# Kernel tuning notes

Hardware: AMD Instinct MI355X
Metric: run time of the kernel (lower is better)

Reference implementation:

```python
import jax, jax.numpy as jnp
import numpy as np

DIM = 1024
NUM_EXPERTS = 8
TOP_K = 2
HIDDEN = DIM * 2
B, S = 2, 4096


def setup_inputs() -> dict:
    key = jax.random.key(0)
    ks = jax.random.split(key, 8)
    sd = 1.0 / np.sqrt(DIM)
    sh = 1.0 / np.sqrt(HIDDEN)
    return {
        "x": jax.random.normal(ks[0], (B, S, DIM), dtype=jnp.float32),
        "gate_w": jax.random.uniform(ks[1], (NUM_EXPERTS, DIM), jnp.float32, -sd, sd),
        "gate_b": jax.random.uniform(ks[2], (NUM_EXPERTS,), jnp.float32, -sd, sd),
        "W1": jax.random.uniform(ks[3], (NUM_EXPERTS, DIM, HIDDEN), jnp.float32, -sd, sd),
        "b1": jax.random.uniform(ks[4], (NUM_EXPERTS, HIDDEN), jnp.float32, -sd, sd),
        "W2": jax.random.uniform(ks[5], (NUM_EXPERTS, HIDDEN, DIM), jnp.float32, -sh, sh),
        "b2": jax.random.uniform(ks[6], (NUM_EXPERTS, DIM), jnp.float32, -sh, sh),
    }


def reference(x, gate_w, gate_b, W1, b1, W2, b2):
    Bd, Sd, D = x.shape
    xf = x.reshape(-1, D)                                  # [T, D]
    T = xf.shape[0]
    logits = xf @ gate_w.T + gate_b                        # [T, E]
    weights = jax.nn.softmax(logits.astype(jnp.float32), axis=-1)
    topk_w, topk_i = jax.lax.top_k(weights, TOP_K)         # [T, K]
    topk_w = topk_w / topk_w.sum(axis=-1, keepdims=True)
    # combine weights scattered back to dense [T, E] (top-k indices are distinct)
    comb = jnp.zeros((T, NUM_EXPERTS), topk_w.dtype)
    comb = comb.at[jnp.arange(T)[:, None], topk_i].add(topk_w)
    # dense all-expert FFN (exact GELU, matching nn.GELU default)
    h = jax.nn.gelu(jnp.einsum('td,edh->eth', xf, W1) + b1[:, None, :], approximate=False)
    y = jnp.einsum('eth,ehd->etd', h, W2) + b2[:, None, :]  # [E, T, D]
    out = jnp.einsum('etd,te->td', y, comb.astype(y.dtype)).reshape(Bd, Sd, D)
    return out, logits
```

## Files before the change

### kernel.cpp

```cpp
#include <hip/hip_runtime.h>
#include <math.h>

#define T_TOK 8192
#define DIMX 1024
#define NE 8
#define HID 2048
#define NPAIR (T_TOK * 2)
#define P_PAD (NPAIR + NE * 128)
#define GATE_TPB 32

typedef __attribute__((ext_vector_type(8))) short s16x8;
typedef __attribute__((ext_vector_type(4))) float f32x4;

static __device__ __forceinline__ unsigned short f2bf(float f) {
    union { float f; unsigned u; } v; v.f = f;
    unsigned r = v.u + 0x7FFFu + ((v.u >> 16) & 1u);
    return (unsigned short)(r >> 16);
}
static __device__ __forceinline__ float bf2f(unsigned short u) {
    union { unsigned u; float f; } v; v.u = (unsigned)u << 16; return v.f;
}

static __device__ __forceinline__ float gelu_fast(float v) {
    float u2 = -1.5957691216057308f * v * (1.f + 0.044715f * v * v);
    return v * __builtin_amdgcn_rcpf(1.f + __expf(u2));
}

static __device__ __forceinline__ void gload16(const unsigned short* g, unsigned short* l) {
    __builtin_amdgcn_global_load_lds(
        (const __attribute__((address_space(1))) unsigned int*)g,
        (__attribute__((address_space(3))) unsigned int*)l, 16, 0, 0);
}

__global__ void init_routing_kernel(int* slot_token, float* slot_weight, int* counts) {
    int i = blockIdx.x * blockDim.x + threadIdx.x;
    if (i < P_PAD) { slot_token[i] = 0; slot_weight[i] = 0.f; }
    if (i < NE) counts[i] = 0;
}

__global__ void convx_kernel(const float* __restrict__ x, unsigned short* __restrict__ xb) {
    int i = blockIdx.x * blockDim.x + threadIdx.x;
    float4 f = ((const float4*)x)[i];
    unsigned short r[4] = { f2bf(f.x), f2bf(f.y), f2bf(f.z), f2bf(f.w) };
    *(uint2*)&xb[(size_t)i * 4] = *(const uint2*)&r[0];
}

__global__ __launch_bounds__(256) void conv_transpose_kernel(
    const float* __restrict__ src, unsigned short* __restrict__ dst, int R, int C) {
    __shared__ float tile[64][65];
    int e = blockIdx.z;
    int r0 = blockIdx.y * 64, c0 = blockIdx.x * 64;
    const float* s = src + (size_t)e * R * C;
    unsigned short* d = dst + (size_t)e * R * C;
    int tid = threadIdx.x;
    int lr = tid >> 4, lc4 = (tid & 15) * 4;
    #pragma unroll
    for (int it = 0; it < 4; it++) {
        float4 v = *(const float4*)&s[(size_t)(r0 + it * 16 + lr) * C + c0 + lc4];
        tile[it * 16 + lr][lc4 + 0] = v.x;
        tile[it * 16 + lr][lc4 + 1] = v.y;
        tile[it * 16 + lr][lc4 + 2] = v.z;
        tile[it * 16 + lr][lc4 + 3] = v.w;
    }
    __syncthreads();
    int cc = tid >> 3, rch = (tid & 7) * 8;
    #pragma unroll
    for (int it = 0; it < 2; it++) {
        int c = it * 32 + cc;
        unsigned short r[8];
        #pragma unroll
        for (int j = 0; j < 8; j++) r[j] = f2bf(tile[rch + j][c]);
        *(uint4*)&d[(size_t)(c0 + c) * R + r0 + rch] = *(const uint4*)&r[0];
    }
}

__global__ __launch_bounds__(256) void gate_kernel(
    const float* __restrict__ x, const float* __restrict__ gw, const float* __restrict__ gb,
    float* __restrict__ logits_out, int* counts, int* __restrict__ pair_epos,
    float* __restrict__ pair_w) {
    __shared__ float sgw[NE * DIMX];
    __shared__ int lcount[NE], lbase[NE];
    __shared__ int s_e[GATE_TPB * 2];
    __shared__ int s_lp[GATE_TPB * 2];
    __shared__ float s_wv[GATE_TPB * 2];
    int tid = threadIdx.x;
    for (int i = tid; i < NE * DIMX / 4; i += 256)
        ((float4*)sgw)[i] = ((const float4*)gw)[i];
    if (tid < NE) lcount[tid] = 0;
    __syncthreads();

    int wave = tid >> 6, lane = tid & 63;
    int tbase = blockIdx.x * GATE_TPB;
    for (int r = 0; r < GATE_TPB / 4; ++r) {
        int ti = wave * (GATE_TPB / 4) + r;
        int t = tbase + ti;
        const float* xr = x + (size_t)t * DIMX;
        float acc[NE] = {};
        #pragma unroll
        for (int i = 0; i < DIMX / 256; i++) {
            float4 xv = *(const float4*)&xr[i * 256 + lane * 4];
            #pragma unroll
            for (int e = 0; e < NE; e++) {
                float4 wv = *(const float4*)&sgw[e * DIMX + i * 256 + lane * 4];
                acc[e] += xv.x * wv.x + xv.y * wv.y + xv.z * wv.z + xv.w * wv.w;
            }
        }
        #pragma unroll
        for (int e = 0; e < NE; e++) {
            #pragma unroll
            for (int off = 32; off; off >>= 1) acc[e] += __shfl_xor(acc[e], off);
        }
        if (lane == 0) {
            float* lo = logits_out + (size_t)t * NE;
            #pragma unroll
            for (int e = 0; e < NE; e++) { acc[e] += gb[e]; lo[e] = acc[e]; }
            float l0 = acc[0]; int e0 = 0;
            #pragma unroll
            for (int e = 1; e < NE; e++) if (acc[e] > l0) { l0 = acc[e]; e0 = e; }
            float l1 = -1e30f; int e1 = -1;
            #pragma unroll
            for (int e = 0; e < NE; e++) if (e != e0 && acc[e] > l1) { l1 = acc[e]; e1 = e; }
            float q = expf(l1 - l0);
            float wn0 = 1.f / (1.f + q);
            float wn1 = q / (1.f + q);
            int lp0 = atomicAdd(&lcount[e0], 1);
            int lp1 = atomicAdd(&lcount[e1], 1);
            s_e[ti * 2] = e0; s_lp[ti * 2] = lp0; s_wv[ti * 2] = wn0;
            s_e[ti * 2 + 1] = e1; s_lp[ti * 2 + 1] = lp1; s_wv[ti * 2 + 1] = wn1;
        }
    }
    __syncthreads();
    if (tid < NE) lbase[tid] = atomicAdd(&counts[tid], lcount[tid]);
    __syncthreads();
    if (tid < GATE_TPB * 2) {
        int e = s_e[tid];
        int gp = lbase[e] + s_lp[tid];
        int gi = (tbase + (tid >> 1)) * 2 + (tid & 1);
        pair_epos[gi] = (e << 28) | gp;
        pair_w[gi] = s_wv[tid];
    }
}

__global__ void scan_kernel(const int* counts, int* offsets) {
    if (threadIdx.x == 0 && blockIdx.x == 0) {
        int o = 0;
        offsets[0] = 0;
        for (int e = 0; e < NE; e++) { o += (counts[e] + 127) & ~127; offsets[e + 1] = o; }
    }
}

__global__ void place_kernel(const int* __restrict__ pair_epos, const float* __restrict__ pair_w,
                             const int* __restrict__ offsets, int* __restrict__ slot_token,
                             float* __restrict__ slot_weight, int* __restrict__ tok2slot) {
    int p = blockIdx.x * 256 + threadIdx.x;
    if (p >= NPAIR) return;
    int ep = pair_epos[p];
    int e = ep >> 28;
    int pos = ep & 0x0FFFFFFF;
    int slot = offsets[e] + pos;
    slot_token[slot] = p >> 1;
    slot_weight[slot] = pair_w[p];
    tok2slot[p] = slot;
}

#define BARRIER() asm volatile("s_barrier" ::: "memory")
#define WAIT_VM(n) asm volatile("s_waitcnt vmcnt(" #n ")" ::: "memory")
#define WAIT_LGKM0() do { asm volatile("s_waitcnt lgkmcnt(0)" ::: "memory"); \
                          __builtin_amdgcn_sched_barrier(0); } while (0)


__global__ __launch_bounds__(256) void gemm1_kernel(
    const unsigned short* __restrict__ xb, const unsigned short* __restrict__ W1t,
    const float* __restrict__ b1, const int* __restrict__ offsets,
    const int* __restrict__ slot_token, unsigned short* __restrict__ hbuf) {
    int e = blockIdx.x;
    int row_base = offsets[e];
    int rows = offsets[e + 1] - row_base;
    int m0 = blockIdx.z * 128;
    if (m0 >= rows) return;
    int n0 = blockIdx.y * 128;

    __shared__ unsigned short sA[3][128 * 32];
    __shared__ unsigned short sB[3][128 * 32];

    int tid = threadIdx.x;
    const unsigned short* w1e = W1t + (size_t)e * HID * DIMX;

    int srow = tid >> 2;
    int kperm = (tid & 3) ^ ((tid >> 3) & 3);
    int tok0 = slot_token[row_base + m0 + srow];
    int tok1 = slot_token[row_base + m0 + srow + 64];
    const unsigned short* gA0 = xb + (size_t)tok0 * DIMX + kperm * 8;
    const unsigned short* gA1 = xb + (size_t)tok1 * DIMX + kperm * 8;
    const unsigned short* gB0 = w1e + (size_t)(n0 + srow) * DIMX + kperm * 8;
    const unsigned short* gB1 = w1e + (size_t)(n0 + srow + 64) * DIMX + kperm * 8;

#define STG1(b, k0) do { \
        gload16(gA0 + (k0), &sA[b][tid * 8]); \
        gload16(gA1 + (k0), &sA[b][(tid + 256) * 8]); \
        gload16(gB0 + (k0), &sB[b][tid * 8]); \
        gload16(gB1 + (k0), &sB[b][(tid + 256) * 8]); \
    } while (0)

    f32x4 acc[4][4] = {};
    int wv = tid >> 6; int wr = wv >> 1, wc = wv & 1;
    int lane = tid & 63; int lr = lane & 15, lg = lane >> 4;
    int kx8 = (lg ^ ((lr >> 1) & 3)) * 8;

#define CMP1(CUR) do { \
        s16x8 af[4], bfr[4]; \
        _Pragma("unroll") \
        for (int m = 0; m < 4; m++) af[m] = *(const s16x8*)&sA[CUR][(wr * 64 + m * 16 + lr) * 32 + kx8]; \
        _Pragma("unroll") \
        for (int n = 0; n < 4; n++) bfr[n] = *(const s16x8*)&sB[CUR][(wc * 64 + n * 16 + lr) * 32 + kx8]; \
        __builtin_amdgcn_s_setprio(1); \
        _Pragma("unroll") \
        for (int m = 0; m < 4; m++) { \
            _Pragma("unroll") \
            for (int n = 0; n < 4; n++) \
                acc[m][n] = __builtin_amdgcn_mfma_f32_16x16x32_bf16(af[m], bfr[n], acc[m][n], 0, 0, 0); \
        } \
        __builtin_amdgcn_s_setprio(0); \
    } while (0)

    const int NT = DIMX / 32;
    STG1(0, 0);
    STG1(1, 32);
    int cur = 0;
    for (int t = 0; t < NT - 2; ++t) {
        int nxt = cur + 2; if (nxt >= 3) nxt -= 3;
        STG1(nxt, (t + 2) * 32);
        WAIT_VM(8);
        BARRIER();
        CMP1(cur);
        WAIT_LGKM0();
        BARRIER();
        cur = (cur + 1 == 3) ? 0 : cur + 1;
    }
    WAIT_VM(4);
    BARRIER();
    CMP1(cur);
    WAIT_LGKM0();
    BARRIER();
    cur = (cur + 1 == 3) ? 0 : cur + 1;
    WAIT_VM(0);
    BARRIER();
    CMP1(cur);
#undef STG1
#undef CMP1

    #pragma unroll
    for (int m = 0; m < 4; m++) {
        #pragma unroll
        for (int n = 0; n < 4; n++) {
            int col = n0 + wc * 64 + n * 16 + lr;
            float bias = b1[e * HID + col];
            #pragma unroll
            for (int i = 0; i < 4; i++) {
                int row = wr * 64 + m * 16 + lg * 4 + i;
                float v = gelu_fast(acc[m][n][i] + bias);
                hbuf[(size_t)(row_base + m0 + row) * HID + col] = f2bf(v);
            }
        }
    }
}

__global__ __launch_bounds__(256) void gemm2_kernel(
    const unsigned short* __restrict__ hbuf, const unsigned short* __restrict__ W2t,
    const float* __restrict__ b2, const int* __restrict__ offsets,
    const float* __restrict__ slot_weight, unsigned short* __restrict__ ybuf) {
    int e = blockIdx.x;
    int row_base = offsets[e];
    int rows = offsets[e + 1] - row_base;
    int m0 = blockIdx.z * 128;
    if (m0 >= rows) return;
    int n0 = blockIdx.y * 128;

    __shared__ unsigned short sA[3][128 * 32];
    __shared__ unsigned short sB[3][128 * 32];
    __shared__ float s_w[128];

    int tid = threadIdx.x;
    if (tid < 128) s_w[tid] = slot_weight[row_base + m0 + tid];

    const unsigned short* ha = hbuf + (size_t)(row_base + m0) * HID;
    const unsigned short* w2e = W2t + (size_t)e * DIMX * HID;

    int srow = tid >> 2;
    int kperm = (tid & 3) ^ ((tid >> 3) & 3);
    const unsigned short* gA0 = ha + (size_t)srow * HID + kperm * 8;
    const unsigned short* gA1 = ha + (size_t)(srow + 64) * HID + kperm * 8;
    const unsigned short* gB0 = w2e + (size_t)(n0 + srow) * HID + kperm * 8;
    const unsigned short* gB1 = w2e + (size_t)(n0 + srow + 64) * HID + kperm * 8;

#define STG2(b, k0) do { \
        gload16(gA0 + (k0), &sA[b][tid * 8]); \
        gload16(gA1 + (k0), &sA[b][(tid + 256) * 8]); \
        gload16(gB0 + (k0), &sB[b][tid * 8]); \
        gload16(gB1 + (k0), &sB[b][(tid + 256) * 8]); \
    } while (0)

    f32x4 acc[4][4] = {};
    int wv = tid >> 6; int wr = wv >> 1, wc = wv & 1;
    int lane = tid & 63; int lr = lane & 15, lg = lane >> 4;
    int kx8 = (lg ^ ((lr >> 1) & 3)) * 8;

#define CMP2(CUR) do { \
        s16x8 af[4], bfr[4]; \
        _Pragma("unroll") \
        for (int m = 0; m < 4; m++) af[m] = *(const s16x8*)&sA[CUR][(wr * 64 + m * 16 + lr) * 32 + kx8]; \
        _Pragma("unroll") \
        for (int n = 0; n < 4; n++) bfr[n] = *(const s16x8*)&sB[CUR][(wc * 64 + n * 16 + lr) * 32 + kx8]; \
        __builtin_amdgcn_s_setprio(1); \
        _Pragma("unroll") \
        for (int m = 0; m < 4; m++) { \
            _Pragma("unroll") \
            for (int n = 0; n < 4; n++) \
                acc[m][n] = __builtin_amdgcn_mfma_f32_16x16x32_bf16(af[m], bfr[n], acc[m][n], 0, 0, 0); \
        } \
        __builtin_amdgcn_s_setprio(0); \
    } while (0)

    const int NT = HID / 32;
    STG2(0, 0);
    STG2(1, 32);
    int cur = 0;
    for (int t = 0; t < NT - 2; ++t) {
        int nxt = cur + 2; if (nxt >= 3) nxt -= 3;
        STG2(nxt, (t + 2) * 32);
        WAIT_VM(8);
        BARRIER();
        CMP2(cur);
        WAIT_LGKM0();
        BARRIER();
        cur = (cur + 1 == 3) ? 0 : cur + 1;
    }
    WAIT_VM(4);
    BARRIER();
    CMP2(cur);
    WAIT_LGKM0();
    BARRIER();
    cur = (cur + 1 == 3) ? 0 : cur + 1;
    WAIT_VM(0);
    BARRIER();
    CMP2(cur);
#undef STG2
#undef CMP2

    #pragma unroll
    for (int m = 0; m < 4; m++) {
        #pragma unroll
        for (int n = 0; n < 4; n++) {
            int col = n0 + wc * 64 + n * 16 + lr;
            float bias = b2[e * DIMX + col];
            #pragma unroll
            for (int i = 0; i < 4; i++) {
                int row = wr * 64 + m * 16 + lg * 4 + i;
                float v = (acc[m][n][i] + bias) * s_w[row];
                ybuf[(size_t)(row_base + m0 + row) * DIMX + col] = f2bf(v);
            }
        }
    }
}

__global__ __launch_bounds__(256) void combine_kernel(
    const unsigned short* __restrict__ ybuf, const int* __restrict__ tok2slot,
    float* __restrict__ out) {
    int t = blockIdx.x;
    int d = threadIdx.x * 4;
    int sa = tok2slot[t * 2], sb = tok2slot[t * 2 + 1];
    ushort4 a = *(const ushort4*)&ybuf[(size_t)sa * DIMX + d];
    ushort4 b = *(const ushort4*)&ybuf[(size_t)sb * DIMX + d];
    float4 o;
    o.x = bf2f(a.x) + bf2f(b.x);
    o.y = bf2f(a.y) + bf2f(b.y);
    o.z = bf2f(a.z) + bf2f(b.z);
    o.w = bf2f(a.w) + bf2f(b.w);
    *(float4*)&out[(size_t)t * DIMX + d] = o;
}

extern "C" void kernel_launch(void* const* d_in, const int* in_sizes, int n_in,
                              void* d_out, int out_size, void* d_ws, size_t ws_size,
                              hipStream_t stream) {
    const float* x  = (const float*)d_in[0];
    const float* gw = (const float*)d_in[1];
    const float* gb = (const float*)d_in[2];
    const float* W1 = (const float*)d_in[3];
    const float* b1 = (const float*)d_in[4];
    const float* W2 = (const float*)d_in[5];
    const float* b2 = (const float*)d_in[6];
    float* out = (float*)d_out;
    float* logits = out + (size_t)T_TOK * DIMX;

    char* ws = (char*)d_ws;
    unsigned short* W2t = (unsigned short*)ws; ws += (size_t)NE * DIMX * HID * 2;
    unsigned short* W1t = (unsigned short*)ws;
    unsigned short* ybuf = (unsigned short*)ws; ws += (size_t)NE * DIMX * HID * 2;
    unsigned short* xb = (unsigned short*)ws; ws += (size_t)T_TOK * DIMX * 2;
    unsigned short* hbuf = (unsigned short*)ws; ws += (size_t)P_PAD * HID * 2;
    int* counts = (int*)ws; ws += 256;
    int* offsets = (int*)ws; ws += 256;
    int* pair_epos = (int*)ws; ws += (size_t)NPAIR * 4;
    float* pair_w = (float*)ws; ws += (size_t)NPAIR * 4;
    int* slot_token = (int*)ws; ws += (size_t)P_PAD * 4;
    float* slot_weight = (float*)ws; ws += (size_t)P_PAD * 4;
    int* tok2slot = (int*)ws; ws += (size_t)NPAIR * 4;

    init_routing_kernel<<<(P_PAD + 255) / 256, 256, 0, stream>>>(slot_token, slot_weight, counts);
    convx_kernel<<<T_TOK * DIMX / 4 / 256, 256, 0, stream>>>(x, xb);
    conv_transpose_kernel<<<dim3(HID / 64, DIMX / 64, NE), 256, 0, stream>>>(W1, W1t, DIMX, HID);
    conv_transpose_kernel<<<dim3(DIMX / 64, HID / 64, NE), 256, 0, stream>>>(W2, W2t, HID, DIMX);
    gate_kernel<<<T_TOK / GATE_TPB, 256, 0, stream>>>(x, gw, gb, logits, counts, pair_epos, pair_w);
    scan_kernel<<<1, 1, 0, stream>>>(counts, offsets);
    place_kernel<<<NPAIR / 256, 256, 0, stream>>>(pair_epos, pair_w, offsets, slot_token,
                                                  slot_weight, tok2slot);
    gemm1_kernel<<<dim3(NE, HID / 128, 128), 256, 0, stream>>>(xb, W1t, b1, offsets, slot_token, hbuf);
    gemm2_kernel<<<dim3(NE, DIMX / 128, 128), 256, 0, stream>>>(hbuf, W2t, b2, offsets, slot_weight, ybuf);
    combine_kernel<<<T_TOK, 256, 0, stream>>>(ybuf, tok2slot, out);
}
```

Measured before the change: 285.4 us.

## Fuse x bf16 conversion into gate kernel and use double-buffered GEMM pipelines

The separate x-to-bf16 conversion kernel is removed; the gate kernel now writes the bf16 copy of x while it already reads x for the gating dot products, saving one launch and one full read of x. Both expert GEMM kernels go from a 3-stage LDS pipeline (two tiles prefetched ahead) to a 2-stage double buffer. That shrinks LDS use, which may allow more resident blocks, but each tile load has less time to hide its latency.

After: 281.0 us. Within noise of the previous version (-1.5%).

```diff
diff --git a/kernel.cpp b/kernel.cpp
--- a/kernel.cpp
+++ b/kernel.cpp
@@ -36,13 +36,6 @@
     int i = blockIdx.x * blockDim.x + threadIdx.x;
     if (i < P_PAD) { slot_token[i] = 0; slot_weight[i] = 0.f; }
     if (i < NE) counts[i] = 0;
-}
-
-__global__ void convx_kernel(const float* __restrict__ x, unsigned short* __restrict__ xb) {
-    int i = blockIdx.x * blockDim.x + threadIdx.x;
-    float4 f = ((const float4*)x)[i];
-    unsigned short r[4] = { f2bf(f.x), f2bf(f.y), f2bf(f.z), f2bf(f.w) };
-    *(uint2*)&xb[(size_t)i * 4] = *(const uint2*)&r[0];
 }
 
 __global__ __launch_bounds__(256) void conv_transpose_kernel(
@@ -77,7 +70,7 @@
 __global__ __launch_bounds__(256) void gate_kernel(
     const float* __restrict__ x, const float* __restrict__ gw, const float* __restrict__ gb,
     float* __restrict__ logits_out, int* counts, int* __restrict__ pair_epos,
-    float* __restrict__ pair_w) {
+    float* __restrict__ pair_w, unsigned short* __restrict__ xb) {
     __shared__ float sgw[NE * DIMX];
     __shared__ int lcount[NE], lbase[NE];
     __shared__ int s_e[GATE_TPB * 2];
@@ -99,6 +92,8 @@
         #pragma unroll
         for (int i = 0; i < DIMX / 256; i++) {
             float4 xv = *(const float4*)&xr[i * 256 + lane * 4];
+            unsigned short rb[4] = { f2bf(xv.x), f2bf(xv.y), f2bf(xv.z), f2bf(xv.w) };
+            *(uint2*)&xb[(size_t)t * DIMX + i * 256 + lane * 4] = *(const uint2*)&rb[0];
             #pragma unroll
             for (int e = 0; e < NE; e++) {
                 float4 wv = *(const float4*)&sgw[e * DIMX + i * 256 + lane * 4];
@@ -180,8 +175,8 @@
     if (m0 >= rows) return;
     int n0 = blockIdx.y * 128;
 
-    __shared__ unsigned short sA[3][128 * 32];
-    __shared__ unsigned short sB[3][128 * 32];
+    __shared__ unsigned short sA[2][128 * 32];
+    __shared__ unsigned short sB[2][128 * 32];
 
     int tid = threadIdx.x;
     const unsigned short* w1e = W1t + (size_t)e * HID * DIMX;
@@ -225,24 +220,16 @@
 
     const int NT = DIMX / 32;
     STG1(0, 0);
-    STG1(1, 32);
     int cur = 0;
-    for (int t = 0; t < NT - 2; ++t) {
-        int nxt = cur + 2; if (nxt >= 3) nxt -= 3;
-        STG1(nxt, (t + 2) * 32);
-        WAIT_VM(8);
+    for (int t = 0; t < NT - 1; ++t) {
+        STG1(cur ^ 1, (t + 1) * 32);
+        WAIT_VM(4);
         BARRIER();
         CMP1(cur);
         WAIT_LGKM0();
         BARRIER();
-        cur = (cur + 1 == 3) ? 0 : cur + 1;
-    }
-    WAIT_VM(4);
-    BARRIER();
-    CMP1(cur);
-    WAIT_LGKM0();
-    BARRIER();
-    cur = (cur + 1 == 3) ? 0 : cur + 1;
+        cur ^= 1;
+    }
     WAIT_VM(0);
     BARRIER();
     CMP1(cur);
@@ -276,8 +263,8 @@
     if (m0 >= rows) return;
     int n0 = blockIdx.y * 128;
 
-    __shared__ unsigned short sA[3][128 * 32];
-    __shared__ unsigned short sB[3][128 * 32];
+    __shared__ unsigned short sA[2][128 * 32];
+    __shared__ unsigned short sB[2][128 * 32];
     __shared__ float s_w[128];
 
     int tid = threadIdx.x;
@@ -323,24 +310,16 @@
 
     const int NT = HID / 32;
     STG2(0, 0);
-    STG2(1, 32);
     int cur = 0;
-    for (int t = 0; t < NT - 2; ++t) {
-        int nxt = cur + 2; if (nxt >= 3) nxt -= 3;
-        STG2(nxt, (t + 2) * 32);
-        WAIT_VM(8);
+    for (int t = 0; t < NT - 1; ++t) {
+        STG2(cur ^ 1, (t + 1) * 32);
+        WAIT_VM(4);
         BARRIER();
         CMP2(cur);
         WAIT_LGKM0();
         BARRIER();
-        cur = (cur + 1 == 3) ? 0 : cur + 1;
-    }
-    WAIT_VM(4);
-    BARRIER();
-    CMP2(cur);
-    WAIT_LGKM0();
-    BARRIER();
-    cur = (cur + 1 == 3) ? 0 : cur + 1;
+        cur ^= 1;
+    }
     WAIT_VM(0);
     BARRIER();
     CMP2(cur);
@@ -407,10 +386,10 @@
     int* tok2slot = (int*)ws; ws += (size_t)NPAIR * 4;
 
     init_routing_kernel<<<(P_PAD + 255) / 256, 256, 0, stream>>>(slot_token, slot_weight, counts);
-    convx_kernel<<<T_TOK * DIMX / 4 / 256, 256, 0, stream>>>(x, xb);
     conv_transpose_kernel<<<dim3(HID / 64, DIMX / 64, NE), 256, 0, stream>>>(W1, W1t, DIMX, HID);
     conv_transpose_kernel<<<dim3(DIMX / 64, HID / 64, NE), 256, 0, stream>>>(W2, W2t, HID, DIMX);
-    gate_kernel<<<T_TOK / GATE_TPB, 256, 0, stream>>>(x, gw, gb, logits, counts, pair_epos, pair_w);
+    gate_kernel<<<T_TOK / GATE_TPB, 256, 0, stream>>>(x, gw, gb, logits, counts, pair_epos,
+                                                      pair_w, xb);
     scan_kernel<<<1, 1, 0, stream>>>(counts, offsets);
     place_kernel<<<NPAIR / 256, 256, 0, stream>>>(pair_epos, pair_w, offsets, slot_token,
                                                   slot_weight, tok2slot);
```
